# Kernel optimization log

Measured on AMD Instinct MI355X. Metric: run time of the kernel, lower is better.

The kernel has to match this reference:

```python
import jax, jax.numpy as jnp
import numpy as np

def setup_inputs() -> dict:
    key = jax.random.key(0)
    k1, k2, k3 = jax.random.split(key, 3)
    B, N, D = 4, 2048, 1024
    x = jax.random.normal(k1, (B, N, D), dtype=jnp.float32)
    # nn.Linear weights are (out_features, in_features); init scale ~1/sqrt(D)
    W_Q = jax.random.normal(k2, (D, D), dtype=jnp.float32) / np.sqrt(D)
    W_K = jax.random.normal(k3, (D, D), dtype=jnp.float32) / np.sqrt(D)
    return {"x": x, "W_Q": W_Q, "W_K": W_K, "n_iters": 5}

def reference(x, W_Q, W_K, n_iters):
    # K = Linear(W_K)(x) = x @ W_K.T  -> (B, N, D)
    K = jnp.einsum('bnd,kd->bnk', x, W_K)
    y = x
    for _ in range(n_iters):
        Q = jnp.einsum('bnd,kd->bnk', y, W_Q)          # (B, N, D)
        scores = jnp.einsum('bnd,bmd->bnm', K, Q)       # K @ Q^T, (B, N, N)
        probs = jax.nn.softmax(scores, axis=-1)
        y = jnp.einsum('bnm,bmd->bnd', probs, x)        # (B, N, D)
    return y
```

## Files before the change

### kernel.cpp

```cpp
#include <hip/hip_runtime.h>
#include <cstdint>

typedef _Float16 f16;
typedef __attribute__((ext_vector_type(8))) _Float16 v8h;
typedef __attribute__((ext_vector_type(4))) float v4f;

#define LO_SCALE 4096.0f
#define LO_INV   2.44140625e-4f

__device__ __forceinline__ void split2(float f, f16& h, f16& l) {
    h = (f16)f;
    l = (f16)((f - (float)h) * LO_SCALE);
}

__device__ __forceinline__ void gload_lds16(const void* g, void* l) {
    __builtin_amdgcn_global_load_lds(
        (const __attribute__((address_space(1))) unsigned int*)(uintptr_t)g,
        (__attribute__((address_space(3))) unsigned int*)(unsigned int)(uintptr_t)l,
        16, 0, 0);
}

__global__ __launch_bounds__(256)
void gemm_nt_2limb(const f16* __restrict__ A1, const f16* __restrict__ A2,
                   const f16* __restrict__ B1, const f16* __restrict__ B2,
                   float* __restrict__ C32, f16* __restrict__ Ch,
                   f16* __restrict__ Cl, int mode, int N, int K)
{
    __shared__ f16 lds[4 * 128 * 32];
    f16* lA1 = lds;
    f16* lA2 = lds + 128 * 32;
    f16* lB1 = lds + 2 * 128 * 32;
    f16* lB2 = lds + 3 * 128 * 32;

    const int tid  = threadIdx.x;
    const int lane = tid & 63;
    const int wave = tid >> 6;
    const int wm = wave >> 1, wn = wave & 1;
    const int fr = lane & 15, quad = lane >> 4;
    const int row0 = blockIdx.y * 128;
    const int col0 = blockIdx.x * 128;
    const int l4 = lane >> 2;
    const int c8 = (lane & 3) * 8;

    v4f accB[4][4], accS[4][4];
#pragma unroll
    for (int i = 0; i < 4; ++i)
#pragma unroll
        for (int j = 0; j < 4; ++j) {
            accB[i][j] = {0.f, 0.f, 0.f, 0.f};
            accS[i][j] = {0.f, 0.f, 0.f, 0.f};
        }

    for (int k0 = 0; k0 < K; k0 += 32) {
#pragma unroll
        for (int t = 0; t < 2; ++t) {
            const int slot = wave + 4 * t;
            const int r = slot * 16 + l4;
            const size_t ga = (size_t)(row0 + r) * K + (k0 + c8);
            const size_t gb = (size_t)(col0 + r) * K + (k0 + c8);
            const unsigned loff = slot * 1024;
            gload_lds16(A1 + ga, (char*)lA1 + loff);
            gload_lds16(A2 + ga, (char*)lA2 + loff);
            gload_lds16(B1 + gb, (char*)lB1 + loff);
            gload_lds16(B2 + gb, (char*)lB2 + loff);
        }
        __syncthreads();

        v8h a1[4], a2[4], b1[4], b2[4];
#pragma unroll
        for (int i = 0; i < 4; ++i) {
            const int off = (wm * 64 + i * 16 + fr) * 32 + quad * 8;
            a1[i] = *(const v8h*)&lA1[off];
            a2[i] = *(const v8h*)&lA2[off];
        }
#pragma unroll
        for (int j = 0; j < 4; ++j) {
            const int off = (wn * 64 + j * 16 + fr) * 32 + quad * 8;
            b1[j] = *(const v8h*)&lB1[off];
            b2[j] = *(const v8h*)&lB2[off];
        }
#pragma unroll
        for (int i = 0; i < 4; ++i)
#pragma unroll
            for (int j = 0; j < 4; ++j) {
                accB[i][j] = __builtin_amdgcn_mfma_f32_16x16x32_f16(a1[i], b1[j], accB[i][j], 0, 0, 0);
                accS[i][j] = __builtin_amdgcn_mfma_f32_16x16x32_f16(a2[i], b1[j], accS[i][j], 0, 0, 0);
                accS[i][j] = __builtin_amdgcn_mfma_f32_16x16x32_f16(a1[i], b2[j], accS[i][j], 0, 0, 0);
            }
        __syncthreads();
    }

#pragma unroll
    for (int i = 0; i < 4; ++i)
#pragma unroll
        for (int j = 0; j < 4; ++j) {
            const int row = row0 + wm * 64 + i * 16 + quad * 4;
            const int col = col0 + wn * 64 + j * 16 + fr;
#pragma unroll
            for (int r = 0; r < 4; ++r) {
                const float v = accB[i][j][r] + accS[i][j][r] * LO_INV;
                const size_t off = (size_t)(row + r) * N + col;
                if (mode == 0) {
                    C32[off] = v;
                } else if (mode == 1) {
                    f16 h, l; split2(v, h, l);
                    Ch[off] = h; Cl[off] = l;
                } else {
                    C32[off] = v;
                    Ch[off] = (f16)v;
                }
            }
        }
}

__global__ __launch_bounds__(512)
void gemm_nt_f16_256(const f16* __restrict__ A, const f16* __restrict__ B,
                     f16* __restrict__ C, int N, int K,
                     size_t sA, size_t sB, size_t sC)
{
    __shared__ f16 lds[2 * 2 * 256 * 64];

    const int bz = blockIdx.z;
    A += (size_t)bz * sA; B += (size_t)bz * sB; C += (size_t)bz * sC;

    const int tid  = threadIdx.x;
    const int lane = tid & 63;
    const int wave = tid >> 6;
    const int wm = wave >> 2;
    const int wn = wave & 3;
    const int fr = lane & 15, quad = lane >> 4;
    const int row0 = blockIdx.y * 256;
    const int col0 = blockIdx.x * 256;
    const int NT = K >> 6;

    const int rsub = tid >> 3;
    const int csub = (((tid & 7) ^ ((tid >> 3) & 7)) * 8);

    auto STAGE = [&](int T) {
        const unsigned bufB = (unsigned)(T & 1) * 65536u;
#pragma unroll
        for (int q = 0; q < 4; ++q) {
            const f16* op = (q >= 2) ? B : A;
            const int r0 = ((q >= 2) ? col0 : row0) + (q & 1) * 128;
#pragma unroll
            for (int t2 = 0; t2 < 2; ++t2) {
                const f16* g = op + (size_t)(r0 + t2 * 64 + rsub) * K + T * 64 + csub;
                gload_lds16(g, (char*)lds + bufB + (unsigned)(q >> 1) * 32768u
                                 + (unsigned)(q & 1) * 16384u
                                 + (unsigned)(t2 * 8192 + wave * 1024));
            }
        }
    };

    auto LRD = [&](const f16* base, int row, int ks) {
        return *(const v8h*)&base[row * 64 + (((ks * 4 + quad) ^ (row & 7)) * 8)];
    };

    v4f acc[8][4];
#pragma unroll
    for (int i = 0; i < 8; ++i)
#pragma unroll
        for (int j = 0; j < 4; ++j)
            acc[i][j] = {0.f, 0.f, 0.f, 0.f};

    STAGE(0);
    asm volatile("s_waitcnt vmcnt(0)" ::: "memory");
    __builtin_amdgcn_s_barrier();

    for (int t = 0; t < NT; ++t) {
        const int bc = (t & 1) * 32768;
        const f16* lA = lds + bc;
        const f16* lB = lds + bc + 16384;

        v8h bfr[4][2];
#pragma unroll
        for (int j = 0; j < 4; ++j)
#pragma unroll
            for (int ks = 0; ks < 2; ++ks)
                bfr[j][ks] = LRD(lB, wn * 64 + j * 16 + fr, ks);
        {
            v8h a0[2], a1[2];
#pragma unroll
            for (int ks = 0; ks < 2; ++ks) {
                a0[ks] = LRD(lA, wm * 128 + 0 + fr, ks);
                a1[ks] = LRD(lA, wm * 128 + 16 + fr, ks);
            }
            if (t + 1 < NT) STAGE(t + 1);
            __builtin_amdgcn_s_barrier();
            asm volatile("s_waitcnt lgkmcnt(0)" ::: "memory");
            __builtin_amdgcn_s_setprio(1);
#pragma unroll
            for (int j = 0; j < 4; ++j) {
                acc[0][j] = __builtin_amdgcn_mfma_f32_16x16x32_f16(a0[0], bfr[j][0], acc[0][j], 0, 0, 0);
                acc[0][j] = __builtin_amdgcn_mfma_f32_16x16x32_f16(a0[1], bfr[j][1], acc[0][j], 0, 0, 0);
                acc[1][j] = __builtin_amdgcn_mfma_f32_16x16x32_f16(a1[0], bfr[j][0], acc[1][j], 0, 0, 0);
                acc[1][j] = __builtin_amdgcn_mfma_f32_16x16x32_f16(a1[1], bfr[j][1], acc[1][j], 0, 0, 0);
            }
            __builtin_amdgcn_s_setprio(0);
            __builtin_amdgcn_s_barrier();
        }

#pragma unroll
        for (int p = 1; p < 4; ++p) {
            v8h ap[2][2];
#pragma unroll
            for (int u = 0; u < 2; ++u)
#pragma unroll
                for (int ks = 0; ks < 2; ++ks)
                    ap[u][ks] = LRD(lA, wm * 128 + (p * 2 + u) * 16 + fr, ks);
            __builtin_amdgcn_s_barrier();
            asm volatile("s_waitcnt lgkmcnt(0)" ::: "memory");
            __builtin_amdgcn_s_setprio(1);
#pragma unroll
            for (int u = 0; u < 2; ++u)
#pragma unroll
                for (int j = 0; j < 4; ++j) {
                    acc[p * 2 + u][j] = __builtin_amdgcn_mfma_f32_16x16x32_f16(ap[u][0], bfr[j][0], acc[p * 2 + u][j], 0, 0, 0);
                    acc[p * 2 + u][j] = __builtin_amdgcn_mfma_f32_16x16x32_f16(ap[u][1], bfr[j][1], acc[p * 2 + u][j], 0, 0, 0);
                }
            __builtin_amdgcn_s_setprio(0);
            if (p == 3)
                asm volatile("s_waitcnt vmcnt(0)" ::: "memory");
            __builtin_amdgcn_s_barrier();
        }
    }

#pragma unroll
    for (int i = 0; i < 8; ++i)
#pragma unroll
        for (int j = 0; j < 4; ++j) {
            const int row = row0 + wm * 128 + i * 16 + quad * 4;
            const int col = col0 + wn * 64 + j * 16 + fr;
#pragma unroll
            for (int r = 0; r < 4; ++r)
                C[(size_t)(row + r) * N + col] = (f16)acc[i][j][r];
        }
}

__global__ __launch_bounds__(256)
void split_f32(const float* __restrict__ in, f16* __restrict__ h,
               f16* __restrict__ l, int n)
{
    const int i = (blockIdx.x * 256 + threadIdx.x) * 4;
    if (i >= n) return;
    const float4 v = *(const float4*)(in + i);
    f16 hh[4], ll[4];
    split2(v.x, hh[0], ll[0]);
    split2(v.y, hh[1], ll[1]);
    split2(v.z, hh[2], ll[2]);
    split2(v.w, hh[3], ll[3]);
    *(ushort4*)(h + i) = *(const ushort4*)hh;
    *(ushort4*)(l + i) = *(const ushort4*)ll;
}

__global__ __launch_bounds__(256)
void transpose_split(const float* __restrict__ in, f16* __restrict__ oh,
                     f16* __restrict__ ol, int R, int C)
{
    __shared__ float tile[32][33];
    const int tx = threadIdx.x & 31, ty = threadIdx.x >> 5;
    const int ic = blockIdx.x * 32 + tx;
    const int ir = blockIdx.y * 32 + ty;
#pragma unroll
    for (int k = 0; k < 32; k += 8)
        tile[ty + k][tx] = in[(size_t)(ir + k) * C + ic];
    __syncthreads();
    const int oc  = blockIdx.y * 32 + tx;
    const int orr = blockIdx.x * 32 + ty;
#pragma unroll
    for (int k = 0; k < 32; k += 8) {
        f16 h, l;
        split2(tile[tx][ty + k], h, l);
        oh[(size_t)(orr + k) * R + oc] = h;
        ol[(size_t)(orr + k) * R + oc] = l;
    }
}

#define CAP 1024

__global__ __launch_bounds__(256)
void refine_pv(const f16* __restrict__ S, const float* __restrict__ Kt,
               const float* __restrict__ Y, const float* __restrict__ X,
               float* __restrict__ Yout, f16* __restrict__ Yh)
{
    const int r = blockIdx.x;
    const int b = r >> 11;
    const int t = threadIdx.x;
    const int wave = t >> 6, lane = t & 63;

    __shared__ float red[4];
    __shared__ int cnt;
    __shared__ int idxs[CAP + 8];
    __shared__ float ex[CAP + 8];

    float s[8];
    {
        const v8h sv = *(const v8h*)(S + (size_t)r * 2048 + t * 8);
#pragma unroll
        for (int k = 0; k < 8; ++k) s[k] = (float)sv[k];
    }
    float m = s[0];
#pragma unroll
    for (int k = 1; k < 8; ++k) m = fmaxf(m, s[k]);
#pragma unroll
    for (int off = 32; off > 0; off >>= 1) m = fmaxf(m, __shfl_xor(m, off));
    if (lane == 0) red[wave] = m;
    if (t == 0) cnt = 0;
    __syncthreads();
    m = fmaxf(fmaxf(red[0], red[1]), fmaxf(red[2], red[3]));

    const float thresh = m - 18.0f;
#pragma unroll
    for (int k = 0; k < 8; ++k)
        if (s[k] > thresh) {
            const int p = atomicAdd(&cnt, 1);
            if (p < CAP) idxs[p] = t * 8 + k;
        }
    __syncthreads();
    const int count = min(cnt, CAP);

    const float* krow  = Kt + (size_t)r * 1024;
    const float* ybase = Y + (size_t)b * 2048 * 1024;
    for (int j = wave; j < count; j += 4) {
        const float* yrow = ybase + (size_t)idxs[j] * 1024;
        float acc = 0.f;
#pragma unroll
        for (int d = 0; d < 4; ++d) {
            const int e = lane * 4 + d * 256;
            const float4 kv = *(const float4*)(krow + e);
            const float4 yv = *(const float4*)(yrow + e);
            acc += kv.x * yv.x + kv.y * yv.y + kv.z * yv.z + kv.w * yv.w;
        }
#pragma unroll
        for (int off = 32; off > 0; off >>= 1) acc += __shfl_xor(acc, off);
        if (lane == 0) ex[j] = acc;
    }
    __syncthreads();

    float lm = -3.0e38f;
    for (int j = t; j < count; j += 256) lm = fmaxf(lm, ex[j]);
#pragma unroll
    for (int off = 32; off > 0; off >>= 1) lm = fmaxf(lm, __shfl_xor(lm, off));
    if (lane == 0) red[wave] = lm;
    __syncthreads();
    const float M2 = fmaxf(fmaxf(red[0], red[1]), fmaxf(red[2], red[3]));
    __syncthreads();

    float ls = 0.f;
    for (int j = t; j < count; j += 256) {
        const float e = expf(ex[j] - M2);
        ex[j] = e;
        ls += e;
    }
#pragma unroll
    for (int off = 32; off > 0; off >>= 1) ls += __shfl_xor(ls, off);
    if (lane == 0) red[wave] = ls;
    __syncthreads();
    const float inv = 1.0f / (red[0] + red[1] + red[2] + red[3]);
    for (int j = t; j < count; j += 256) ex[j] *= inv;
    const int countPad = (count + 7) & ~7;
    if (t < countPad - count) {
        ex[count + t]   = 0.f;
        idxs[count + t] = 0;
    }
    __syncthreads();

    const float* xb = X + (size_t)b * 2048 * 1024;
    float4 acc = {0.f, 0.f, 0.f, 0.f};
    for (int j = 0; j < countPad; j += 8) {
        float4 v[8];
        float  pw[8];
#pragma unroll
        for (int k = 0; k < 8; ++k) {
            pw[k] = ex[j + k];
            v[k] = *(const float4*)(xb + (size_t)idxs[j + k] * 1024 + t * 4);
        }
#pragma unroll
        for (int k = 0; k < 8; ++k) {
            acc.x += pw[k] * v[k].x;
            acc.y += pw[k] * v[k].y;
            acc.z += pw[k] * v[k].z;
            acc.w += pw[k] * v[k].w;
        }
    }
    const size_t o = (size_t)r * 1024 + t * 4;
    *(float4*)(Yout + o) = acc;
    f16 h[4] = {(f16)acc.x, (f16)acc.y, (f16)acc.z, (f16)acc.w};
    *(ushort4*)(Yh + o) = *(const ushort4*)h;
}

extern "C" void kernel_launch(void* const* d_in, const int* in_sizes, int n_in,
                              void* d_out, int out_size, void* d_ws, size_t ws_size,
                              hipStream_t stream)
{
    const float* x  = (const float*)d_in[0];
    const float* Wq = (const float*)d_in[1];
    const float* Wk = (const float*)d_in[2];
    const int n_iters = 5;

    const size_t NXe = 8388608;
    const size_t NWe = 1048576;
    const size_t NSe = 16777216;
    const size_t NR  = 8192;

    char* p = (char*)d_ws;
    f16* xh   = (f16*)p; p += NXe * 2;
    f16* xl   = (f16*)p; p += NXe * 2;
    f16* wkth = (f16*)p; p += NWe * 2;
    f16* wktl = (f16*)p; p += NWe * 2;
    f16* wqth = (f16*)p; p += NWe * 2;
    f16* wqtl = (f16*)p; p += NWe * 2;
    f16* vth  = (f16*)p; p += NWe * 2;
    f16* vtl  = (f16*)p; p += NWe * 2;
    float* kt32 = (float*)p; p += NXe * 4;
    f16*  kt16  = (f16*)p;  p += NXe * 2;
    f16*  st    = (f16*)p;  p += NSe * 2;
    f16*  yh    = (f16*)p;  p += NXe * 2;
    float* y1   = (float*)p; p += NXe * 4;
    float* y2   = (float*)p; p += NXe * 4;
    if ((size_t)(p - (char*)d_ws) > ws_size) return;

    float* out = (float*)d_out;

    split_f32<<<dim3(NXe / 1024), dim3(256), 0, stream>>>(x, xh, xl, (int)NXe);
    transpose_split<<<dim3(32, 32), dim3(256), 0, stream>>>(Wk, wkth, wktl, 1024, 1024);
    transpose_split<<<dim3(32, 32), dim3(256), 0, stream>>>(Wq, wqth, wqtl, 1024, 1024);
    gemm_nt_2limb<<<dim3(8, 8), dim3(256), 0, stream>>>(
        wqth, wqtl, wkth, wktl, nullptr, vth, vtl, 1, 1024, 1024);
    gemm_nt_2limb<<<dim3(8, 64), dim3(256), 0, stream>>>(
        xh, xl, vth, vtl, kt32, kt16, nullptr, 2, 1024, 1024);

    const float* yr = x;
    float* pingpong[2] = {y1, y2};
    for (int it = 0; it < n_iters; ++it) {
        float* yw = (it == n_iters - 1) ? out : pingpong[it & 1];
        const f16* Bop = (it == 0) ? xh : yh;
        gemm_nt_f16_256<<<dim3(8, 8, 4), dim3(512), 0, stream>>>(
            kt16, Bop, st, 2048, 1024,
            (size_t)2048 * 1024, (size_t)2048 * 1024, (size_t)2048 * 2048);
        refine_pv<<<dim3(NR), dim3(256), 0, stream>>>(
            st, kt32, yr, x, yw, yh);
        yr = yw;
    }
}
```

Before: 769.2 us.

## Add 256x128-tile two-limb GEMM with LDS double buffering for K projection

Adds a specialized two-limb fp16 GEMM that uses 512 threads, 256x128 output tiles, swizzled LDS layout and direct global-to-LDS double-buffered loads. It replaces the 8x64 grid launch of the generic kernel for the x·V projection. It also remaps block IDs so neighbouring blocks share operands in cache. This runs once outside the iteration loop, so it targets only the setup GEMM. The cost is larger LDS use and lower occupancy per block.

```diff
diff --git a/kernel.cpp b/kernel.cpp
--- a/kernel.cpp
+++ b/kernel.cpp
@@ -109,6 +109,135 @@
                     C32[off] = v;
                     Ch[off] = (f16)v;
                 }
+            }
+        }
+}
+
+__global__ __launch_bounds__(512)
+void gemm_nt_2limb_256(const f16* __restrict__ A1, const f16* __restrict__ A2,
+                       const f16* __restrict__ B1, const f16* __restrict__ B2,
+                       float* __restrict__ C32, f16* __restrict__ Ch,
+                       int N, int K)
+{
+    __shared__ f16 lds[2 * 24576];
+
+    const int bid = blockIdx.x;
+    const int lid = (bid & 7) * 32 + (bid >> 3);
+    const int col0 = (lid & 7) * 128;
+    const int row0 = (lid >> 3) * 256;
+
+    const int tid  = threadIdx.x;
+    const int lane = tid & 63;
+    const int wave = tid >> 6;
+    const int wm = wave >> 1;
+    const int wn = wave & 1;
+    const int fr = lane & 15, quad = lane >> 4;
+    const int NT = K >> 5;
+
+    const int trow = tid >> 2;
+    const int tchunk = tid & 3;
+
+    auto STAGE = [&](int T) {
+        const unsigned bufB = (unsigned)(T & 1) * 49152u;
+        const int k0 = T * 32;
+#pragma unroll
+        for (int rd = 0; rd < 2; ++rd) {
+            const int r = trow + rd * 128;
+            const int sc = (tchunk ^ ((r >> 1) & 3)) * 8;
+            const size_t ga = (size_t)(row0 + r) * K + k0 + sc;
+            const unsigned dof = (unsigned)(rd * 8192 + wave * 1024);
+            gload_lds16(A1 + ga, (char*)lds + bufB + dof);
+            gload_lds16(A2 + ga, (char*)lds + bufB + 16384u + dof);
+        }
+        {
+            const int r = trow;
+            const int sc = (tchunk ^ ((r >> 1) & 3)) * 8;
+            const size_t gb = (size_t)(col0 + r) * K + k0 + sc;
+            const unsigned dof = (unsigned)(wave * 1024);
+            gload_lds16(B1 + gb, (char*)lds + bufB + 32768u + dof);
+            gload_lds16(B2 + gb, (char*)lds + bufB + 40960u + dof);
+        }
+    };
+
+    auto LRD = [&](const f16* base, int row) {
+        return *(const v8h*)&base[row * 32 + ((quad ^ ((row >> 1) & 3)) * 8)];
+    };
+
+    v4f accB[4][4], accS[4][4];
+#pragma unroll
+    for (int i = 0; i < 4; ++i)
+#pragma unroll
+        for (int j = 0; j < 4; ++j) {
+            accB[i][j] = {0.f, 0.f, 0.f, 0.f};
+            accS[i][j] = {0.f, 0.f, 0.f, 0.f};
+        }
+
+    STAGE(0);
+    asm volatile("s_waitcnt vmcnt(0)" ::: "memory");
+    __builtin_amdgcn_s_barrier();
+
+    for (int t = 0; t < NT; ++t) {
+        const int bc = (t & 1) * 24576;
+        const f16* lA1 = lds + bc;
+        const f16* lA2 = lds + bc + 8192;
+        const f16* lB1 = lds + bc + 16384;
+        const f16* lB2 = lds + bc + 20480;
+
+        v8h b1[4], b2[4];
+#pragma unroll
+        for (int j = 0; j < 4; ++j) {
+            b1[j] = LRD(lB1, wn * 64 + j * 16 + fr);
+            b2[j] = LRD(lB2, wn * 64 + j * 16 + fr);
+        }
+        {
+            v8h a1 = LRD(lA1, wm * 64 + 0 + fr);
+            v8h a2 = LRD(lA2, wm * 64 + 0 + fr);
+            if (t + 1 < NT) STAGE(t + 1);
+            __builtin_amdgcn_s_barrier();
+            asm volatile("s_waitcnt lgkmcnt(0)" ::: "memory");
+            __builtin_amdgcn_s_setprio(1);
+#pragma unroll
+            for (int j = 0; j < 4; ++j) {
+                accB[0][j] = __builtin_amdgcn_mfma_f32_16x16x32_f16(a1, b1[j], accB[0][j], 0, 0, 0);
+                accS[0][j] = __builtin_amdgcn_mfma_f32_16x16x32_f16(a2, b1[j], accS[0][j], 0, 0, 0);
+                accS[0][j] = __builtin_amdgcn_mfma_f32_16x16x32_f16(a1, b2[j], accS[0][j], 0, 0, 0);
+            }
+            __builtin_amdgcn_s_setprio(0);
+            __builtin_amdgcn_s_barrier();
+        }
+
+#pragma unroll
+        for (int p = 1; p < 4; ++p) {
+            v8h a1 = LRD(lA1, wm * 64 + p * 16 + fr);
+            v8h a2 = LRD(lA2, wm * 64 + p * 16 + fr);
+            __builtin_amdgcn_s_barrier();
+            asm volatile("s_waitcnt lgkmcnt(0)" ::: "memory");
+            __builtin_amdgcn_s_setprio(1);
+#pragma unroll
+            for (int j = 0; j < 4; ++j) {
+                accB[p][j] = __builtin_amdgcn_mfma_f32_16x16x32_f16(a1, b1[j], accB[p][j], 0, 0, 0);
+                accS[p][j] = __builtin_amdgcn_mfma_f32_16x16x32_f16(a2, b1[j], accS[p][j], 0, 0, 0);
+                accS[p][j] = __builtin_amdgcn_mfma_f32_16x16x32_f16(a1, b2[j], accS[p][j], 0, 0, 0);
+            }
+            __builtin_amdgcn_s_setprio(0);
+            if (p == 3)
+                asm volatile("s_waitcnt vmcnt(0)" ::: "memory");
+            __builtin_amdgcn_s_barrier();
+        }
+    }
+
+#pragma unroll
+    for (int i = 0; i < 4; ++i)
+#pragma unroll
+        for (int j = 0; j < 4; ++j) {
+            const int row = row0 + wm * 64 + i * 16 + quad * 4;
+            const int col = col0 + wn * 64 + j * 16 + fr;
+#pragma unroll
+            for (int r = 0; r < 4; ++r) {
+                const float v = accB[i][j][r] + accS[i][j][r] * LO_INV;
+                const size_t off = (size_t)(row + r) * N + col;
+                C32[off] = v;
+                Ch[off] = (f16)v;
             }
         }
 }
@@ -427,8 +556,8 @@
     transpose_split<<<dim3(32, 32), dim3(256), 0, stream>>>(Wq, wqth, wqtl, 1024, 1024);
     gemm_nt_2limb<<<dim3(8, 8), dim3(256), 0, stream>>>(
         wqth, wqtl, wkth, wktl, nullptr, vth, vtl, 1, 1024, 1024);
-    gemm_nt_2limb<<<dim3(8, 64), dim3(256), 0, stream>>>(
-        xh, xl, vth, vtl, kt32, kt16, nullptr, 2, 1024, 1024);
+    gemm_nt_2limb_256<<<dim3(256), dim3(512), 0, stream>>>(
+        xh, xl, vth, vtl, kt32, kt16, 1024, 1024);
 
     const float* yr = x;
     float* pingpong[2] = {y1, y2};
```

Result: faster. 729.0 us (-5.2%).
